# Performance work log

Hardware: AMD Instinct MI355X
Metric: run time of the kernel (lower is better)

The kernel has to match this reference:

```python
import jax, jax.numpy as jnp
import numpy as np

KERNEL = 3          # conv kernel size (stride 1)
NUM_SEG = 512       # static cap on number of pooled segments (pad semantics)
NEG = -10.0         # fill value for positions not covered by the strided conv


def _sinusoidal_pe(S, D):
    pos = np.arange(S)[:, None].astype(np.float32)
    div = np.exp(-np.log(10000.0) * (np.arange(0, D, 2).astype(np.float32) / D))
    pe = np.zeros((S, D), dtype=np.float32)
    pe[:, 0::2] = np.sin(pos * div)
    pe[:, 1::2] = np.cos(pos * div)
    return jnp.asarray(pe)


def setup_inputs() -> dict:
    key = jax.random.key(0)
    B, L, D = 8, 2048, 1024
    Ch = D // KERNEL  # 341
    ks = jax.random.split(key, 4)
    hidden = jax.random.normal(ks[0], (B, L, D), jnp.float32)
    lengths = jax.random.randint(ks[1], (B,), L // 2, L + 1)
    attention_mask = (jnp.arange(L)[None, :] < lengths[:, None]).astype(jnp.float32)
    w1 = jax.random.normal(ks[2], (Ch, D, KERNEL), jnp.float32) / np.sqrt(D * KERNEL)
    b1 = jnp.zeros((Ch,), jnp.float32)
    w2 = jax.random.normal(ks[3], (1, Ch, 1), jnp.float32) / np.sqrt(Ch)
    b2 = jnp.full((1,), -2.5, jnp.float32)  # init_for_12 bias
    return {"hidden": hidden, "attention_mask": attention_mask,
            "w1": w1, "b1": b1, "w2": w2, "b2": b2}


def reference(hidden, attention_mask, w1, b1, w2, b2):
    B, L, D = hidden.shape
    dt = hidden.dtype
    # --- strided-conv boundary logits (eval path, no Gumbel noise) ---
    x = jnp.swapaxes(hidden, 1, 2)  # (B, D, L)
    h = jax.lax.conv_general_dilated(x, w1, (1,), 'VALID',
                                     dimension_numbers=('NCH', 'OIH', 'NCH'))
    h = jax.nn.relu(h + b1[None, :, None])            # (B, Ch, L-2)
    strided = jnp.einsum('bcl,oc->bl', h, w2[:, :, 0]) + b2[0]  # (B, L-2)
    # scatter strided logits to positions kernel-1 + i (i.e. [2:L])
    logits = jnp.full((B, L), NEG, dt).at[:, KERNEL - 1:].set(strided)
    probs = jax.nn.sigmoid(logits)
    soft = probs
    hard_samp = (probs > 0.5).astype(dt)
    hard = hard_samp + soft - jax.lax.stop_gradient(soft)  # straight-through
    # --- mask and force a boundary at the last real token ---
    hard = hard * attention_mask
    pad = attention_mask == 0
    first_pad = pad & (jnp.cumsum(pad.astype(jnp.int32), axis=1) == 1)
    last_real = jnp.roll(first_pad, -1, axis=1).at[:, -1].set(False).astype(dt)
    hard = jnp.maximum(hard, last_real)
    # --- dynamic downsample: mean-pool tokens within boundary segments ---
    seg = jnp.cumsum(hard, axis=1) - hard  # segment id per token (B, L)
    sid = jnp.arange(NUM_SEG, dtype=dt)
    foo = 1.0 - jnp.clip(jnp.abs(sid[None, None, :] - seg[:, :, None]), 0.0, 1.0)  # (B,L,S)
    foo = foo * attention_mask[:, :, None]
    lel = foo / (jnp.sum(foo, axis=1, keepdims=True) + 1e-9)
    pooled = jnp.einsum('bls,bld->bsd', lel, hidden)  # (B, S, D)
    pooled = pooled + _sinusoidal_pe(NUM_SEG, D)[None].astype(dt)
    # --- shortened attention mask (stream compaction of kept positions) ---
    keep = jax.lax.stop_gradient(hard) > 0.5
    order = jnp.argsort(jnp.logical_not(keep).astype(jnp.int32), axis=1)  # stable: kept first
    gathered = jnp.take_along_axis(attention_mask, order, axis=1)[:, :NUM_SEG]
    n_keep = jnp.sum(keep, axis=1)
    valid = jnp.arange(NUM_SEG)[None, :] < n_keep[:, None]
    short_mask = jnp.where(valid, gathered, 0.0)
    num_boundaries = jnp.sum(hard)
    total_positions = jnp.sum(attention_mask)
    return pooled, num_boundaries, total_positions, short_mask
```

## Files before the change

### kernel.cpp

```cpp
#include <hip/hip_runtime.h>
#include <hip/hip_bf16.h>
#include <cmath>

#define B_SZ 8
#define L_SZ 2048
#define D_SZ 1024
#define CH 341
#define CP 384
#define LCONV 2046
#define NSEG 512
#define KDIM 3072
#define KSTEPS 48
#define NCHUNK 128
#define NSLOT 640

#define POOLED_N (B_SZ * NSEG * D_SZ)
#define HID_BLOCKS 8192
#define W1_BLOCKS 4608

typedef _Float16 f16x8 __attribute__((ext_vector_type(8)));
typedef float f32x4 __attribute__((ext_vector_type(4)));

__device__ __forceinline__ void gl_lds16(const void* g, void* l) {
    __builtin_amdgcn_global_load_lds(
        (const __attribute__((address_space(1))) unsigned int*)g,
        (__attribute__((address_space(3))) unsigned int*)l, 16, 0, 0);
}

__global__ __launch_bounds__(256) void convert_all_kernel(
        const float* __restrict__ hidden, _Float16* __restrict__ hid16,
        const float* __restrict__ w1, const float* __restrict__ b2,
        _Float16* __restrict__ bfrag, float* __restrict__ logits) {
    if (blockIdx.x < HID_BLOCKS) {
        size_t idx = (size_t)blockIdx.x * 256 + threadIdx.x;
        float4 v0 = ((const float4*)hidden)[idx * 2];
        float4 v1 = ((const float4*)hidden)[idx * 2 + 1];
        f16x8 o;
        o[0] = (_Float16)v0.x; o[1] = (_Float16)v0.y;
        o[2] = (_Float16)v0.z; o[3] = (_Float16)v0.w;
        o[4] = (_Float16)v1.x; o[5] = (_Float16)v1.y;
        o[6] = (_Float16)v1.z; o[7] = (_Float16)v1.w;
        ((f16x8*)hid16)[idx] = o;
    } else {
        int idx = (blockIdx.x - HID_BLOCKS) * 256 + threadIdx.x;
        int j = idx & 7;
        int lane = (idx >> 3) & 63;
        int kc = (idx >> 9) & 1;
        int rest = idx >> 10;
        int s = rest % KSTEPS;
        int tt = rest / KSTEPS;
        int c = tt * 16 + (lane & 15);
        int k = s * 64 + kc * 32 + ((lane >> 4) << 3) + j;
        int kk = k >> 10, d = k & 1023;
        float v = (c < CH) ? w1[((size_t)c * 1024 + d) * 3 + kk] : 0.0f;
        bfrag[idx] = (_Float16)v;
        if (idx < B_SZ * LCONV) logits[idx] = b2[0];
    }
}

#define LDS_BUF 8192

__global__ __launch_bounds__(256, 2) void conv_mfma_kernel(
        const _Float16* __restrict__ hid16, const _Float16* __restrict__ bfrag,
        const float* __restrict__ b1, const float* __restrict__ w2,
        float* __restrict__ logits) {
    const int nt = blockIdx.x;
    const int mt = blockIdx.y;
    const int b  = blockIdx.z;
    const int l0 = mt * 64;
    const int n0 = nt * 192;
    const int tid = threadIdx.x;
    const int wave = tid >> 6, lane = tid & 63;
    const int wn = wave;
    const int quad = lane >> 4, l16 = lane & 15;

    __shared__ __align__(16) char lds[2 * LDS_BUF];

    const _Float16* hb = hid16 + (size_t)b * L_SZ * D_SZ;

    const _Float16* pa[2];
    #pragma unroll
    for (int p = 0; p < 2; ++p) {
        int f = p * 256 + tid;
        int kc = f >> 8, e = f & 255;
        int m = ((e >> 6) << 4) + (e & 15);
        int koff = ((e >> 4) & 3) * 8;
        int l = l0 + m; if (l > LCONV - 1) l = LCONV - 1;
        pa[p] = hb + (size_t)l * 1024 + kc * 32 + koff;
    }

    const f16x8* bp = (const f16x8*)bfrag;
    const f16x8* bptr[3];
    #pragma unroll
    for (int jj = 0; jj < 3; ++jj) {
        int tt = nt * 12 + wn * 3 + jj;
        bptr[jj] = bp + (size_t)tt * (KSTEPS * 2 * 64) + lane;
    }

    f32x4 acc[4][3] = {};
    f16x8 bc[3][2], bn[3][2];

    #pragma unroll
    for (int jj = 0; jj < 3; ++jj)
        #pragma unroll
        for (int kc = 0; kc < 2; ++kc)
            bc[jj][kc] = bptr[jj][kc * 64];
    #pragma unroll
    for (int jj = 0; jj < 3; ++jj) bptr[jj] += 128;
    #pragma unroll
    for (int p = 0; p < 2; ++p)
        gl_lds16(pa[p], lds + (p * 256 + wave * 64) * 16);
    #pragma unroll
    for (int p = 0; p < 2; ++p) pa[p] += 64;
    __syncthreads();

    int cur = 0;
    for (int s = 0; s < KSTEPS - 1; ++s) {
        const int nxt = cur ^ LDS_BUF;
        #pragma unroll
        for (int jj = 0; jj < 3; ++jj)
            #pragma unroll
            for (int kc = 0; kc < 2; ++kc)
                bn[jj][kc] = bptr[jj][kc * 64];
        #pragma unroll
        for (int jj = 0; jj < 3; ++jj) bptr[jj] += 128;
        #pragma unroll
        for (int p = 0; p < 2; ++p)
            gl_lds16(pa[p], lds + nxt + (p * 256 + wave * 64) * 16);
        #pragma unroll
        for (int p = 0; p < 2; ++p) pa[p] += 64;

        #pragma unroll
        for (int kc = 0; kc < 2; ++kc) {
            f16x8 a[4];
            #pragma unroll
            for (int ii = 0; ii < 4; ++ii)
                a[ii] = *(const f16x8*)(lds + cur + (kc * 256 + ii * 64 + lane) * 16);
            #pragma unroll
            for (int ii = 0; ii < 4; ++ii)
                #pragma unroll
                for (int jj = 0; jj < 3; ++jj)
                    acc[ii][jj] = __builtin_amdgcn_mfma_f32_16x16x32_f16(
                        a[ii], bc[jj][kc], acc[ii][jj], 0, 0, 0);
        }
        __syncthreads();
        #pragma unroll
        for (int jj = 0; jj < 3; ++jj)
            #pragma unroll
            for (int kc = 0; kc < 2; ++kc)
                bc[jj][kc] = bn[jj][kc];
        cur = nxt;
    }
    #pragma unroll
    for (int kc = 0; kc < 2; ++kc) {
        f16x8 a[4];
        #pragma unroll
        for (int ii = 0; ii < 4; ++ii)
            a[ii] = *(const f16x8*)(lds + cur + (kc * 256 + ii * 64 + lane) * 16);
        #pragma unroll
        for (int ii = 0; ii < 4; ++ii)
            #pragma unroll
            for (int jj = 0; jj < 3; ++jj)
                acc[ii][jj] = __builtin_amdgcn_mfma_f32_16x16x32_f16(
                    a[ii], bc[jj][kc], acc[ii][jj], 0, 0, 0);
    }
    __syncthreads();

    float cb1[3], cw2[3];
    #pragma unroll
    for (int jj = 0; jj < 3; ++jj) {
        int ch = n0 + wn * 48 + jj * 16 + l16;
        bool v = ch < CH;
        cb1[jj] = v ? b1[ch] : 0.0f;
        cw2[jj] = v ? w2[ch] : 0.0f;
    }
    float* red = (float*)lds;
    #pragma unroll
    for (int ii = 0; ii < 4; ++ii)
        #pragma unroll
        for (int r = 0; r < 4; ++r) {
            float P = 0.0f;
            #pragma unroll
            for (int jj = 0; jj < 3; ++jj) {
                float h = acc[ii][jj][r] + cb1[jj];
                if (h > 0.0f) P += h * cw2[jj];
            }
            P += __shfl_xor(P, 1);
            P += __shfl_xor(P, 2);
            P += __shfl_xor(P, 4);
            P += __shfl_xor(P, 8);
            if (l16 == 0)
                red[(ii * 16 + quad * 4 + r) * 4 + wn] = P;
        }
    __syncthreads();
    if (tid < 64) {
        int l = l0 + tid;
        if (l < LCONV)
            atomicAdd(&logits[b * LCONV + l],
                      red[tid * 4] + red[tid * 4 + 1] + red[tid * 4 + 2] + red[tid * 4 + 3]);
    }
}

__global__ __launch_bounds__(256) void scanfix_kernel(
        const float* __restrict__ logits, const float* __restrict__ amask,
        const float* __restrict__ hidden, const float* __restrict__ w1,
        const float* __restrict__ b1, const float* __restrict__ w2,
        const float* __restrict__ b2,
        int* __restrict__ segstart, int* __restrict__ segid,
        float* __restrict__ scratch, float* __restrict__ short_mask) {
    const int b = blockIdx.x, tid = threadIdx.x;
    __shared__ float slog[2048];
    __shared__ float hrow[3 * 1024];
    __shared__ int sdata[256];
    __shared__ float sred[256];
    __shared__ int flags[64];
    __shared__ int nflag;
    __shared__ int s_len, s_total;

    for (int t = tid; t < LCONV; t += 256)
        slog[t] = logits[b * LCONV + t];
    if (tid == 0) nflag = 0;

    int cnt = 0;
    #pragma unroll
    for (int j = 0; j < 8; ++j) {
        int l = tid * 8 + j;
        cnt += (amask[b * L_SZ + l] > 0.5f) ? 1 : 0;
    }
    sdata[tid] = cnt; __syncthreads();
    for (int off = 128; off > 0; off >>= 1) {
        if (tid < off) sdata[tid] += sdata[tid + off];
        __syncthreads();
    }
    if (tid == 0) s_len = sdata[0];
    __syncthreads();
    const int len = s_len;

    for (int t = tid; t < LCONV; t += 256)
        if (fabsf(slog[t]) < 0.02f) {
            int k = atomicAdd(&nflag, 1);
            if (k < 64) flags[k] = t;
        }
    __syncthreads();
    const int nf = (nflag < 64) ? nflag : 64;
    for (int fi = 0; fi < nf; ++fi) {
        const int l = flags[fi];
        for (int t = tid; t < 3072; t += 256)
            hrow[t] = hidden[((size_t)b * L_SZ + l) * 1024 + t];
        __syncthreads();
        float tot = 0.0f;
        for (int c = tid; c < CH; c += 256) {
            const float* wr = w1 + (size_t)c * 3072;
            float dot = 0.0f;
            for (int d = 0; d < 1024; ++d)
                dot += hrow[d] * wr[d * 3] + hrow[1024 + d] * wr[d * 3 + 1]
                     + hrow[2048 + d] * wr[d * 3 + 2];
            float h = dot + b1[c];
            if (h > 0.0f) tot += h * w2[c];
        }
        sred[tid] = tot; __syncthreads();
        for (int off = 128; off > 0; off >>= 1) {
            if (tid < off) sred[tid] += sred[tid + off];
            __syncthreads();
        }
        if (tid == 0) slog[l] = sred[0] + b2[0];
        __syncthreads();
    }

    int bits[8]; int tsum = 0;
    #pragma unroll
    for (int j = 0; j < 8; ++j) {
        int l = tid * 8 + j;
        int h = 0;
        if (l >= 2 && l < len) h = (slog[l - 2] > 0.0f) ? 1 : 0;
        if (len < L_SZ && l == len - 1) h = 1;
        bits[j] = h; tsum += h;
    }
    __syncthreads();
    sdata[tid] = tsum; __syncthreads();
    for (int off = 1; off < 256; off <<= 1) {
        int v = (tid >= off) ? sdata[tid - off] : 0;
        __syncthreads();
        sdata[tid] += v;
        __syncthreads();
    }
    const int texcl = sdata[tid] - tsum;
    if (tid == 255) s_total = sdata[255];
    __syncthreads();
    const int total = s_total;

    for (int s = tid; s <= NSEG; s += 256)
        segstart[b * (NSEG + 1) + s] = (s == 0) ? 0 : len;
    __syncthreads();
    int run = texcl;
    #pragma unroll
    for (int j = 0; j < 8; ++j) {
        int l = tid * 8 + j;
        int sv = -1;
        if (l < len && run < NSEG) sv = run;
        segid[b * L_SZ + l] = sv;
        if (bits[j]) {
            if (run + 1 <= NSEG) segstart[b * (NSEG + 1) + run + 1] = l + 1;
            run++;
        }
    }

    if (tid == 0) {
        scratch[b] = (float)total;
        scratch[B_SZ + b] = (float)len;
    }
    for (int s = tid; s < NSEG; s += 256)
        short_mask[b * NSEG + s] = (s < total) ? 1.0f : 0.0f;
}

__global__ __launch_bounds__(256) void pool_partial_kernel(
        const float* __restrict__ hidden, const int* __restrict__ segid,
        float* __restrict__ runsum) {
    const int c = blockIdx.x, b = blockIdx.y;
    const int tid = threadIdx.x;
    const int d0 = tid * 4;
    const int lbase = c * 16;
    const float* hb = hidden + (size_t)b * L_SZ * D_SZ + d0;
    const int* sg = segid + b * L_SZ + lbase;
    float* rb = runsum + ((size_t)(b * NSLOT + c)) * D_SZ + d0;
    float4 acc = make_float4(0.f, 0.f, 0.f, 0.f);
    int cur = -1;
    #pragma unroll
    for (int t = 0; t < 16; ++t) {
        int sid = sg[t];
        if (sid != cur) {
            if (cur >= 0)
                *(float4*)(rb + (size_t)cur * D_SZ) = acc;
            acc = make_float4(0.f, 0.f, 0.f, 0.f);
            cur = sid;
        }
        if (sid >= 0) {
            float4 v = *(const float4*)(hb + (size_t)(lbase + t) * D_SZ);
            acc.x += v.x; acc.y += v.y; acc.z += v.z; acc.w += v.w;
        }
    }
    if (cur >= 0)
        *(float4*)(rb + (size_t)cur * D_SZ) = acc;
}

__global__ __launch_bounds__(256) void pool_gather_kernel(
        const float* __restrict__ runsum, const int* __restrict__ segstart,
        const float* __restrict__ scratch, float* __restrict__ pooled,
        float* __restrict__ out_nb, float* __restrict__ out_tp) {
    const int s = blockIdx.x, b = blockIdx.y, tid = threadIdx.x;
    if (s == 0 && b == 0 && tid == 0) {
        float nb = 0.f, tp = 0.f;
        #pragma unroll
        for (int i = 0; i < B_SZ; ++i) { nb += scratch[i]; tp += scratch[B_SZ + i]; }
        *out_nb = nb; *out_tp = tp;
    }
    const int l0 = segstart[b * (NSEG + 1) + s];
    const int l1 = segstart[b * (NSEG + 1) + s + 1];
    const int d0 = tid * 4;
    float4 a0 = make_float4(0.f, 0.f, 0.f, 0.f);
    float4 a1 = make_float4(0.f, 0.f, 0.f, 0.f);
    if (l1 > l0) {
        const int c0 = l0 >> 4, c1 = (l1 - 1) >> 4;
        const float* rs = runsum + ((size_t)(b * NSLOT + s)) * D_SZ + d0;
        int c = c0;
        for (; c + 1 <= c1; c += 2) {
            float4 v0 = *(const float4*)(rs + (size_t)c * D_SZ);
            float4 v1 = *(const float4*)(rs + (size_t)(c + 1) * D_SZ);
            a0.x += v0.x; a0.y += v0.y; a0.z += v0.z; a0.w += v0.w;
            a1.x += v1.x; a1.y += v1.y; a1.z += v1.z; a1.w += v1.w;
        }
        if (c <= c1) {
            float4 v0 = *(const float4*)(rs + (size_t)c * D_SZ);
            a0.x += v0.x; a0.y += v0.y; a0.z += v0.z; a0.w += v0.w;
        }
    }
    const float inv = 1.0f / ((float)(l1 - l0) + 1e-9f);
    const float ce = -9.210340371976184f / 512.0f;
    const int i = d0 >> 1;
    const float t0 = (float)s * expf(ce * (float)i);
    const float t1 = (float)s * expf(ce * (float)(i + 1));
    float4 out;
    out.x = (a0.x + a1.x) * inv + sinf(t0);
    out.y = (a0.y + a1.y) * inv + cosf(t0);
    out.z = (a0.z + a1.z) * inv + sinf(t1);
    out.w = (a0.w + a1.w) * inv + cosf(t1);
    *(float4*)(pooled + ((size_t)(b * NSEG + s)) * D_SZ + d0) = out;
}

extern "C" void kernel_launch(void* const* d_in, const int* in_sizes, int n_in,
                              void* d_out, int out_size, void* d_ws, size_t ws_size,
                              hipStream_t stream) {
    const float* hidden = (const float*)d_in[0];
    const float* amask  = (const float*)d_in[1];
    const float* w1     = (const float*)d_in[2];
    const float* b1     = (const float*)d_in[3];
    const float* w2     = (const float*)d_in[4];
    const float* b2     = (const float*)d_in[5];

    float* out    = (float*)d_out;
    float* pooled = out;
    float* nb     = out + POOLED_N;
    float* tp     = nb + 1;
    float* smask  = out + POOLED_N + 2;

    const size_t HID_E = (size_t)B_SZ * L_SZ * D_SZ;
    const size_t OFF_HID16    = 0;
    const size_t OFF_BPACK    = OFF_HID16 + HID_E * 2;
    const size_t OFF_LOGITS   = OFF_BPACK + (size_t)CP * KDIM * 2;
    const size_t OFF_SEGSTART = OFF_LOGITS + (size_t)B_SZ * LCONV * 4;
    const size_t OFF_SEGID    = OFF_SEGSTART + (size_t)B_SZ * (NSEG + 1) * 4;
    const size_t OFF_SCRATCH  = OFF_SEGID + (size_t)B_SZ * L_SZ * 4;

    _Float16* hid16  = (_Float16*)((char*)d_ws + OFF_HID16);
    _Float16* bfrag  = (_Float16*)((char*)d_ws + OFF_BPACK);
    float*    logits = (float*)((char*)d_ws + OFF_LOGITS);
    int*      segst  = (int*)((char*)d_ws + OFF_SEGSTART);
    int*      segid  = (int*)((char*)d_ws + OFF_SEGID);
    float*    scratch= (float*)((char*)d_ws + OFF_SCRATCH);
    float*    runsum = (float*)((char*)d_ws + OFF_HID16);

    convert_all_kernel<<<HID_BLOCKS + W1_BLOCKS, 256, 0, stream>>>(
        hidden, hid16, w1, b2, bfrag, logits);
    conv_mfma_kernel<<<dim3(2, 32, B_SZ), 256, 0, stream>>>(hid16, bfrag, b1, w2, logits);
    scanfix_kernel<<<B_SZ, 256, 0, stream>>>(logits, amask, hidden, w1, b1, w2, b2,
                                             segst, segid, scratch, smask);
    pool_partial_kernel<<<dim3(NCHUNK, B_SZ), 256, 0, stream>>>(hidden, segid, runsum);
    pool_gather_kernel<<<dim3(NSEG, B_SZ), 256, 0, stream>>>(runsum, segst, scratch,
                                                             pooled, nb, tp);
}
```

Before: 203.3 us.

## Replace segmented pooling pass with chunk prefix sums computed during fp16 conversion

The fp16 conversion kernel now also sums each 16-row chunk of hidden. The scan kernel builds per-batch prefix sums over those chunks, and the gather kernel computes each segment mean as a prefix difference plus partial-chunk edge rows read directly from hidden. This removes the separate pool_partial pass and the segid writes, which cost one full extra read of hidden. In exchange, the 8 scan blocks now serially walk 128 chunks each, long segments may lose some fp32 precision in the prefix subtraction, and edge rows are re-read from global memory.

```diff
diff --git a/kernel.cpp b/kernel.cpp
--- a/kernel.cpp
+++ b/kernel.cpp
@@ -12,13 +12,12 @@
 #define KDIM 3072
 #define KSTEPS 48
 #define NCHUNK 128
-#define NSLOT 640
+#define W1XB 576
 
 #define POOLED_N (B_SZ * NSEG * D_SZ)
-#define HID_BLOCKS 8192
-#define W1_BLOCKS 4608
 
 typedef _Float16 f16x8 __attribute__((ext_vector_type(8)));
+typedef _Float16 f16x4 __attribute__((ext_vector_type(4)));
 typedef float f32x4 __attribute__((ext_vector_type(4)));
 
 __device__ __forceinline__ void gl_lds16(const void* g, void* l) {
@@ -30,19 +29,27 @@
 __global__ __launch_bounds__(256) void convert_all_kernel(
         const float* __restrict__ hidden, _Float16* __restrict__ hid16,
         const float* __restrict__ w1, const float* __restrict__ b2,
-        _Float16* __restrict__ bfrag, float* __restrict__ logits) {
-    if (blockIdx.x < HID_BLOCKS) {
-        size_t idx = (size_t)blockIdx.x * 256 + threadIdx.x;
-        float4 v0 = ((const float4*)hidden)[idx * 2];
-        float4 v1 = ((const float4*)hidden)[idx * 2 + 1];
-        f16x8 o;
-        o[0] = (_Float16)v0.x; o[1] = (_Float16)v0.y;
-        o[2] = (_Float16)v0.z; o[3] = (_Float16)v0.w;
-        o[4] = (_Float16)v1.x; o[5] = (_Float16)v1.y;
-        o[6] = (_Float16)v1.z; o[7] = (_Float16)v1.w;
-        ((f16x8*)hid16)[idx] = o;
+        _Float16* __restrict__ bfrag, float* __restrict__ logits,
+        float* __restrict__ chunksum) {
+    const int bx = blockIdx.x, b = blockIdx.y;
+    const int tid = threadIdx.x;
+    if (bx < NCHUNK) {
+        const int d0 = tid * 4;
+        const float* src = hidden + ((size_t)b * L_SZ + bx * 16) * D_SZ + d0;
+        _Float16* dst = hid16 + ((size_t)b * L_SZ + bx * 16) * D_SZ + d0;
+        float4 acc = make_float4(0.f, 0.f, 0.f, 0.f);
+        #pragma unroll
+        for (int r = 0; r < 16; ++r) {
+            float4 v = *(const float4*)(src + (size_t)r * D_SZ);
+            acc.x += v.x; acc.y += v.y; acc.z += v.z; acc.w += v.w;
+            f16x4 o;
+            o[0] = (_Float16)v.x; o[1] = (_Float16)v.y;
+            o[2] = (_Float16)v.z; o[3] = (_Float16)v.w;
+            *(f16x4*)(dst + (size_t)r * D_SZ) = o;
+        }
+        *(float4*)(chunksum + ((size_t)(b * NCHUNK + bx)) * D_SZ + d0) = acc;
     } else {
-        int idx = (blockIdx.x - HID_BLOCKS) * 256 + threadIdx.x;
+        int idx = (((bx - NCHUNK) * B_SZ) + b) * 256 + tid;
         int j = idx & 7;
         int lane = (idx >> 3) & 63;
         int kc = (idx >> 9) & 1;
@@ -206,8 +213,9 @@
         const float* __restrict__ hidden, const float* __restrict__ w1,
         const float* __restrict__ b1, const float* __restrict__ w2,
         const float* __restrict__ b2,
-        int* __restrict__ segstart, int* __restrict__ segid,
-        float* __restrict__ scratch, float* __restrict__ short_mask) {
+        int* __restrict__ segstart, float* __restrict__ scratch,
+        float* __restrict__ short_mask,
+        const float* __restrict__ chunksum, float* __restrict__ prefix) {
     const int b = blockIdx.x, tid = threadIdx.x;
     __shared__ float slog[2048];
     __shared__ float hrow[3 * 1024];
@@ -296,9 +304,6 @@
     #pragma unroll
     for (int j = 0; j < 8; ++j) {
         int l = tid * 8 + j;
-        int sv = -1;
-        if (l < len && run < NSEG) sv = run;
-        segid[b * L_SZ + l] = sv;
         if (bits[j]) {
             if (run + 1 <= NSEG) segstart[b * (NSEG + 1) + run + 1] = l + 1;
             run++;
@@ -311,41 +316,34 @@
     }
     for (int s = tid; s < NSEG; s += 256)
         short_mask[b * NSEG + s] = (s < total) ? 1.0f : 0.0f;
-}
-
-__global__ __launch_bounds__(256) void pool_partial_kernel(
-        const float* __restrict__ hidden, const int* __restrict__ segid,
-        float* __restrict__ runsum) {
-    const int c = blockIdx.x, b = blockIdx.y;
-    const int tid = threadIdx.x;
-    const int d0 = tid * 4;
-    const int lbase = c * 16;
-    const float* hb = hidden + (size_t)b * L_SZ * D_SZ + d0;
-    const int* sg = segid + b * L_SZ + lbase;
-    float* rb = runsum + ((size_t)(b * NSLOT + c)) * D_SZ + d0;
-    float4 acc = make_float4(0.f, 0.f, 0.f, 0.f);
-    int cur = -1;
-    #pragma unroll
-    for (int t = 0; t < 16; ++t) {
-        int sid = sg[t];
-        if (sid != cur) {
-            if (cur >= 0)
-                *(float4*)(rb + (size_t)cur * D_SZ) = acc;
-            acc = make_float4(0.f, 0.f, 0.f, 0.f);
-            cur = sid;
-        }
-        if (sid >= 0) {
-            float4 v = *(const float4*)(hb + (size_t)(lbase + t) * D_SZ);
-            acc.x += v.x; acc.y += v.y; acc.z += v.z; acc.w += v.w;
-        }
-    }
-    if (cur >= 0)
-        *(float4*)(rb + (size_t)cur * D_SZ) = acc;
+
+    {
+        const int d0 = tid * 4;
+        const float* cs = chunksum + ((size_t)b * NCHUNK) * D_SZ + d0;
+        float* Pb = prefix + ((size_t)b * (NCHUNK + 1)) * D_SZ + d0;
+        float4 p = make_float4(0.f, 0.f, 0.f, 0.f);
+        *(float4*)Pb = p;
+        for (int c = 0; c < NCHUNK; c += 4) {
+            float4 v0 = *(const float4*)(cs + (size_t)c * D_SZ);
+            float4 v1 = *(const float4*)(cs + (size_t)(c + 1) * D_SZ);
+            float4 v2 = *(const float4*)(cs + (size_t)(c + 2) * D_SZ);
+            float4 v3 = *(const float4*)(cs + (size_t)(c + 3) * D_SZ);
+            p.x += v0.x; p.y += v0.y; p.z += v0.z; p.w += v0.w;
+            *(float4*)(Pb + (size_t)(c + 1) * D_SZ) = p;
+            p.x += v1.x; p.y += v1.y; p.z += v1.z; p.w += v1.w;
+            *(float4*)(Pb + (size_t)(c + 2) * D_SZ) = p;
+            p.x += v2.x; p.y += v2.y; p.z += v2.z; p.w += v2.w;
+            *(float4*)(Pb + (size_t)(c + 3) * D_SZ) = p;
+            p.x += v3.x; p.y += v3.y; p.z += v3.z; p.w += v3.w;
+            *(float4*)(Pb + (size_t)(c + 4) * D_SZ) = p;
+        }
+    }
 }
 
 __global__ __launch_bounds__(256) void pool_gather_kernel(
-        const float* __restrict__ runsum, const int* __restrict__ segstart,
-        const float* __restrict__ scratch, float* __restrict__ pooled,
+        const float* __restrict__ hidden, const float* __restrict__ prefix,
+        const int* __restrict__ segstart, const float* __restrict__ scratch,
+        float* __restrict__ pooled,
         float* __restrict__ out_nb, float* __restrict__ out_tp) {
     const int s = blockIdx.x, b = blockIdx.y, tid = threadIdx.x;
     if (s == 0 && b == 0 && tid == 0) {
@@ -357,21 +355,30 @@
     const int l0 = segstart[b * (NSEG + 1) + s];
     const int l1 = segstart[b * (NSEG + 1) + s + 1];
     const int d0 = tid * 4;
-    float4 a0 = make_float4(0.f, 0.f, 0.f, 0.f);
-    float4 a1 = make_float4(0.f, 0.f, 0.f, 0.f);
+    float4 a = make_float4(0.f, 0.f, 0.f, 0.f);
     if (l1 > l0) {
-        const int c0 = l0 >> 4, c1 = (l1 - 1) >> 4;
-        const float* rs = runsum + ((size_t)(b * NSLOT + s)) * D_SZ + d0;
-        int c = c0;
-        for (; c + 1 <= c1; c += 2) {
-            float4 v0 = *(const float4*)(rs + (size_t)c * D_SZ);
-            float4 v1 = *(const float4*)(rs + (size_t)(c + 1) * D_SZ);
-            a0.x += v0.x; a0.y += v0.y; a0.z += v0.z; a0.w += v0.w;
-            a1.x += v1.x; a1.y += v1.y; a1.z += v1.z; a1.w += v1.w;
-        }
-        if (c <= c1) {
-            float4 v0 = *(const float4*)(rs + (size_t)c * D_SZ);
-            a0.x += v0.x; a0.y += v0.y; a0.z += v0.z; a0.w += v0.w;
+        const int cF = (l0 + 15) >> 4;
+        const int cL = l1 >> 4;
+        const float* hb = hidden + (size_t)b * L_SZ * D_SZ + d0;
+        if (cL > cF) {
+            const float* Pb = prefix + ((size_t)b * (NCHUNK + 1)) * D_SZ + d0;
+            float4 pl = *(const float4*)(Pb + (size_t)cL * D_SZ);
+            float4 pf = *(const float4*)(Pb + (size_t)cF * D_SZ);
+            a.x = pl.x - pf.x; a.y = pl.y - pf.y;
+            a.z = pl.z - pf.z; a.w = pl.w - pf.w;
+            for (int l = l0; l < cF * 16; ++l) {
+                float4 v = *(const float4*)(hb + (size_t)l * D_SZ);
+                a.x += v.x; a.y += v.y; a.z += v.z; a.w += v.w;
+            }
+            for (int l = cL * 16; l < l1; ++l) {
+                float4 v = *(const float4*)(hb + (size_t)l * D_SZ);
+                a.x += v.x; a.y += v.y; a.z += v.z; a.w += v.w;
+            }
+        } else {
+            for (int l = l0; l < l1; ++l) {
+                float4 v = *(const float4*)(hb + (size_t)l * D_SZ);
+                a.x += v.x; a.y += v.y; a.z += v.z; a.w += v.w;
+            }
         }
     }
     const float inv = 1.0f / ((float)(l1 - l0) + 1e-9f);
@@ -380,10 +387,10 @@
     const float t0 = (float)s * expf(ce * (float)i);
     const float t1 = (float)s * expf(ce * (float)(i + 1));
     float4 out;
-    out.x = (a0.x + a1.x) * inv + sinf(t0);
-    out.y = (a0.y + a1.y) * inv + cosf(t0);
-    out.z = (a0.z + a1.z) * inv + sinf(t1);
-    out.w = (a0.w + a1.w) * inv + cosf(t1);
+    out.x = a.x * inv + sinf(t0);
+    out.y = a.y * inv + cosf(t0);
+    out.z = a.z * inv + sinf(t1);
+    out.w = a.w * inv + cosf(t1);
     *(float4*)(pooled + ((size_t)(b * NSEG + s)) * D_SZ + d0) = out;
 }
 
@@ -408,23 +415,23 @@
     const size_t OFF_BPACK    = OFF_HID16 + HID_E * 2;
     const size_t OFF_LOGITS   = OFF_BPACK + (size_t)CP * KDIM * 2;
     const size_t OFF_SEGSTART = OFF_LOGITS + (size_t)B_SZ * LCONV * 4;
-    const size_t OFF_SEGID    = OFF_SEGSTART + (size_t)B_SZ * (NSEG + 1) * 4;
-    const size_t OFF_SCRATCH  = OFF_SEGID + (size_t)B_SZ * L_SZ * 4;
-
-    _Float16* hid16  = (_Float16*)((char*)d_ws + OFF_HID16);
-    _Float16* bfrag  = (_Float16*)((char*)d_ws + OFF_BPACK);
-    float*    logits = (float*)((char*)d_ws + OFF_LOGITS);
-    int*      segst  = (int*)((char*)d_ws + OFF_SEGSTART);
-    int*      segid  = (int*)((char*)d_ws + OFF_SEGID);
-    float*    scratch= (float*)((char*)d_ws + OFF_SCRATCH);
-    float*    runsum = (float*)((char*)d_ws + OFF_HID16);
-
-    convert_all_kernel<<<HID_BLOCKS + W1_BLOCKS, 256, 0, stream>>>(
-        hidden, hid16, w1, b2, bfrag, logits);
+    const size_t OFF_SCRATCH  = OFF_SEGSTART + (size_t)B_SZ * (NSEG + 1) * 4;
+    const size_t OFF_CHUNKSUM = OFF_SCRATCH + 1024;
+    const size_t OFF_PREFIX   = OFF_CHUNKSUM + (size_t)B_SZ * NCHUNK * D_SZ * 4;
+
+    _Float16* hid16   = (_Float16*)((char*)d_ws + OFF_HID16);
+    _Float16* bfrag   = (_Float16*)((char*)d_ws + OFF_BPACK);
+    float*    logits  = (float*)((char*)d_ws + OFF_LOGITS);
+    int*      segst   = (int*)((char*)d_ws + OFF_SEGSTART);
+    float*    scratch = (float*)((char*)d_ws + OFF_SCRATCH);
+    float*    chsum   = (float*)((char*)d_ws + OFF_CHUNKSUM);
+    float*    prefix  = (float*)((char*)d_ws + OFF_PREFIX);
+
+    convert_all_kernel<<<dim3(NCHUNK + W1XB, B_SZ), 256, 0, stream>>>(
+        hidden, hid16, w1, b2, bfrag, logits, chsum);
     conv_mfma_kernel<<<dim3(2, 32, B_SZ), 256, 0, stream>>>(hid16, bfrag, b1, w2, logits);
     scanfix_kernel<<<B_SZ, 256, 0, stream>>>(logits, amask, hidden, w1, b1, w2, b2,
-                                             segst, segid, scratch, smask);
-    pool_partial_kernel<<<dim3(NCHUNK, B_SZ), 256, 0, stream>>>(hidden, segid, runsum);
-    pool_gather_kernel<<<dim3(NSEG, B_SZ), 256, 0, stream>>>(runsum, segst, scratch,
-                                                             pooled, nb, tp);
-}
+                                             segst, scratch, smask, chsum, prefix);
+    pool_gather_kernel<<<dim3(NSEG, B_SZ), 256, 0, stream>>>(hidden, prefix, segst,
+                                                             scratch, pooled, nb, tp);
+}
```

New measurement: 196.8 us. 3.2% less time.
